# Kernel optimization log

Measured on AMD Instinct MI355X. Metric: run time of the kernel, lower is better.

Reference implementation:

```python
import jax, jax.numpy as jnp
import numpy as np

B, M, D, H, DH = 4, 2048, 1024, 16, 64
R_ATTN, FFN_D, R_FFN = 32, 4096, 512
ROPE_THETA = 10000.0
LN_EPS = 1e-5


def layernorm(x, w, b):
    mu = jnp.mean(x, axis=-1, keepdims=True)
    var = jnp.mean(jnp.square(x - mu), axis=-1, keepdims=True)
    return (x - mu) * jax.lax.rsqrt(var + LN_EPS) * w + b


def headwise_svd(x, U, V, b):
    # x: [B,M,D]; U: [H,D,r]; V: [H,r,dh] -> [B,M,H,dh]
    xr = jnp.einsum('bmd,hdr->bmhr', x, U)
    y = jnp.einsum('bmhr,hrk->bmhk', xr, V)
    return y + b.reshape(U.shape[0], -1)


def rotate_half(x):
    x1, x2 = jnp.split(x, 2, axis=-1)
    return jnp.concatenate([-x2, x1], axis=-1)


def rope_cos_sin(m, dh, dtype):
    inv_freq = 1.0 / (ROPE_THETA ** (jnp.arange(0, dh, 2, dtype=jnp.float32) / dh))
    freqs = jnp.arange(m, dtype=jnp.float32)[:, None] * inv_freq[None, :]  # [M, dh/2]
    emb = jnp.concatenate([freqs, freqs], axis=-1)  # [M, dh]
    return jnp.cos(emb).astype(dtype), jnp.sin(emb).astype(dtype)


def setup_inputs() -> dict:
    key = jax.random.key(0)
    ks = jax.random.split(key, 16)
    s = 0.02
    def n(k, shape, scale=s):
        return jax.random.normal(k, shape, dtype=jnp.float32) * scale
    return dict(
        hidden_states=jax.random.normal(ks[0], (B, M, D), dtype=jnp.float32),
        attention_mask=jnp.ones((B, M), dtype=jnp.int32),
        ln1_w=jnp.ones((D,), jnp.float32), ln1_b=jnp.zeros((D,), jnp.float32),
        Uq=n(ks[1], (H, D, R_ATTN)), Vq=n(ks[2], (H, R_ATTN, DH)), bq=jnp.zeros((D,), jnp.float32),
        Uk=n(ks[3], (H, D, R_ATTN)), Vk=n(ks[4], (H, R_ATTN, DH)), bk=jnp.zeros((D,), jnp.float32),
        Uv=n(ks[5], (H, D, R_ATTN)), Vv=n(ks[6], (H, R_ATTN, DH)), bv=jnp.zeros((D,), jnp.float32),
        Wo_attn=n(ks[7], (D, D)), bo_attn=jnp.zeros((D,), jnp.float32),
        ln2_w=jnp.ones((D,), jnp.float32), ln2_b=jnp.zeros((D,), jnp.float32),
        U_wi=n(ks[8], (D, R_FFN)), V_wi=n(ks[9], (R_FFN, 2 * FFN_D)), b_wi=jnp.zeros((2 * FFN_D,), jnp.float32),
        U_wo=n(ks[10], (FFN_D, R_FFN)), V_wo=n(ks[11], (R_FFN, D)), b_wo=jnp.zeros((D,), jnp.float32),
    )


def reference(hidden_states, attention_mask, ln1_w, ln1_b,
              Uq, Vq, bq, Uk, Vk, bk, Uv, Vv, bv,
              Wo_attn, bo_attn, ln2_w, ln2_b,
              U_wi, V_wi, b_wi, U_wo, V_wo, b_wo):
    x = hidden_states
    xn = layernorm(x, ln1_w, ln1_b)

    # head-wise low-rank SVD QKV projections -> [B,H,M,dh]
    q = headwise_svd(xn, Uq, Vq, bq).transpose(0, 2, 1, 3)
    k = headwise_svd(xn, Uk, Vk, bk).transpose(0, 2, 1, 3)
    v = headwise_svd(xn, Uv, Vv, bv).transpose(0, 2, 1, 3)

    cos, sin = rope_cos_sin(x.shape[1], q.shape[-1], q.dtype)  # [M, dh], broadcasts
    q = q * cos + rotate_half(q) * sin
    k = k * cos + rotate_half(k) * sin

    scale = 1.0 / jnp.sqrt(jnp.asarray(q.shape[-1], q.dtype))
    scores = jnp.einsum('bhqd,bhkd->bhqk', q, k) * scale
    pad = (attention_mask == 0)[:, None, None, :]  # [B,1,1,M]
    scores = jnp.where(pad, jnp.finfo(scores.dtype).min, scores)
    attn = jax.nn.softmax(scores, axis=-1)
    ctx = jnp.einsum('bhqk,bhkd->bhqd', attn, v)
    ctx = ctx.transpose(0, 2, 1, 3).reshape(x.shape)  # [B,M,D]
    attn_out = jnp.einsum('bmd,ed->bme', ctx, Wo_attn) + bo_attn  # dense Wo (torch Linear)
    x = x + attn_out

    # FFN: low-rank Wi -> GEGLU(tanh) -> low-rank Wo
    xn2 = layernorm(x, ln2_w, ln2_b)
    h = (xn2 @ U_wi) @ V_wi + b_wi  # [B,M,2*FFN_D]
    h1, h2 = jnp.split(h, 2, axis=-1)
    g = jax.nn.gelu(h1, approximate=True) * h2  # GEGLU, tanh approx
    ffn_out = (g @ U_wo) @ V_wo + b_wo
    return x + ffn_out
```

## Files before the change

kernel.cpp:

```cpp
#include <hip/hip_runtime.h>
#include <cstdint>

#define DEV __device__ __forceinline__

typedef __attribute__((ext_vector_type(8))) short bf16x8;
typedef __attribute__((ext_vector_type(4))) float f32x4;
typedef __attribute__((ext_vector_type(16))) float f32x16;

#define MFMA(a,b,c) __builtin_amdgcn_mfma_f32_16x16x32_bf16((a),(b),(c),0,0,0)
#define MFMA32(a,b,c) __builtin_amdgcn_mfma_f32_32x32x16_bf16((a),(b),(c),0,0,0)

DEV unsigned short f2bf(float f) {
  union { float f; unsigned u; } v; v.f = f;
  unsigned r = v.u + 0x7fffu + ((v.u >> 16) & 1u);
  return (unsigned short)(r >> 16);
}
DEV float bf2f(unsigned short s) {
  union { unsigned u; float f; } v; v.u = ((unsigned)s) << 16; return v.f;
}
DEV float max3f(float a, float b, float c) { return fmaxf(fmaxf(a, b), c); }

DEV void gload16(const unsigned short* g, short* l) {
  __builtin_amdgcn_global_load_lds(
      (const __attribute__((address_space(1))) unsigned*)g,
      (__attribute__((address_space(3))) unsigned*)l, 16, 0, 0);
}


__global__ __launch_bounds__(256) void k_build_wqkv(
    const float* __restrict__ Uq, const float* __restrict__ Vq,
    const float* __restrict__ Uk, const float* __restrict__ Vk,
    const float* __restrict__ Uv, const float* __restrict__ Vv,
    unsigned short* __restrict__ W) {
  __shared__ float Vl[32 * 64];
  int bx = blockIdx.x;
  int proj = bx >> 6;
  int rem = bx & 63;
  int h = rem >> 2, dblk = rem & 3;
  int tid = threadIdx.x;
  int d = dblk * 256 + tid;
  const float* U = (proj == 0) ? Uq : (proj == 1) ? Uk : Uv;
  const float* V = (proj == 0) ? Vq : (proj == 1) ? Vk : Vv;
  {
    const float4* src = (const float4*)(V + (size_t)h * 2048);
    float4* dst = (float4*)Vl;
    dst[tid] = src[tid];
    dst[tid + 256] = src[tid + 256];
  }
  float u[32];
  {
    const float4* ur = (const float4*)(U + ((size_t)h * 1024 + d) * 32);
#pragma unroll
    for (int q = 0; q < 8; ++q) {
      float4 v = ur[q];
      u[q * 4] = v.x; u[q * 4 + 1] = v.y; u[q * 4 + 2] = v.z; u[q * 4 + 3] = v.w;
    }
  }
  __syncthreads();
  unsigned short* wbase = W + ((size_t)(proj * 1024 + h * 64)) * 1024 + d;
  for (int k = 0; k < 64; ++k) {
    float s = 0.f;
#pragma unroll
    for (int r = 0; r < 32; ++r) s += u[r] * Vl[r * 64 + k];
    wbase[(size_t)k * 1024] = f2bf(s);
  }
}

__global__ void k_concat_bias(const float* __restrict__ bq, const float* __restrict__ bk,
                              const float* __restrict__ bv, float* __restrict__ out) {
  int i = blockIdx.x * 256 + threadIdx.x;
  if (i < 1024) out[i] = bq[i];
  else if (i < 2048) out[i] = bk[i - 1024];
  else if (i < 3072) out[i] = bv[i - 2048];
}

__global__ void k_f2bf(const float* __restrict__ in, unsigned short* __restrict__ out, int n) {
  int i = blockIdx.x * 256 + threadIdx.x;
  if (i < n) out[i] = f2bf(in[i]);
}

__global__ void k_transpose_bf16(const float* __restrict__ in, unsigned short* __restrict__ out,
                                 int R, int C) {
  __shared__ float tile[32][33];
  int c0 = blockIdx.x * 32, r0 = blockIdx.y * 32;
  int tx = threadIdx.x, ty = threadIdx.y;
#pragma unroll
  for (int i = ty; i < 32; i += 8)
    tile[i][tx] = in[(size_t)(r0 + i) * C + c0 + tx];
  __syncthreads();
#pragma unroll
  for (int i = ty; i < 32; i += 8)
    out[(size_t)(c0 + i) * R + r0 + tx] = f2bf(tile[tx][i]);
}

__global__ __launch_bounds__(256) void k_vtrans(const unsigned short* __restrict__ qkv,
                                                unsigned short* __restrict__ vT) {
  __shared__ short t[64][66];
  int bh = blockIdx.y, b = bh >> 4, h = bh & 15;
  int m0 = blockIdx.x << 6;
  int tid = threadIdx.x;
  int rr = tid >> 2, cc = (tid & 3) << 4;
  const unsigned short* src = qkv + ((size_t)(b * 2048 + m0 + rr)) * 3072 + 2048 + h * 64 + cc;
  *(bf16x8*)&t[rr][cc] = *(const bf16x8*)src;
  *(bf16x8*)&t[rr][cc + 8] = *(const bf16x8*)(src + 8);
  __syncthreads();
  unsigned short* dst = vT + ((size_t)bh * 64 + rr) * 2048 + m0 + cc;
  bf16x8 o0, o1;
#pragma unroll
  for (int j = 0; j < 8; ++j) o0[j] = t[cc + j][rr];
#pragma unroll
  for (int j = 0; j < 8; ++j) o1[j] = t[cc + 8 + j][rr];
  *(bf16x8*)dst = o0;
  *(bf16x8*)(dst + 8) = o1;
}

__global__ __launch_bounds__(256) void k_layernorm(const float* __restrict__ x,
                                                   const float* __restrict__ w,
                                                   const float* __restrict__ b,
                                                   unsigned short* __restrict__ out) {
  int row = blockIdx.x;
  int tid = threadIdx.x;
  int lane = tid & 63, wid = tid >> 6;
  const float4 v = ((const float4*)(x + (size_t)row * 1024))[tid];
  float s = v.x + v.y + v.z + v.w;
  float s2 = v.x * v.x + v.y * v.y + v.z * v.z + v.w * v.w;
#pragma unroll
  for (int o = 1; o < 64; o <<= 1) { s += __shfl_xor(s, o); s2 += __shfl_xor(s2, o); }
  __shared__ float as_[4], as2_[4];
  if (lane == 0) { as_[wid] = s; as2_[wid] = s2; }
  __syncthreads();
  s = as_[0] + as_[1] + as_[2] + as_[3];
  s2 = as2_[0] + as2_[1] + as2_[2] + as2_[3];
  float mean = s * (1.f / 1024.f);
  float var = s2 * (1.f / 1024.f) - mean * mean;
  float inv = rsqrtf(var + 1e-5f);
  const float4 wv = ((const float4*)w)[tid];
  const float4 bv = ((const float4*)b)[tid];
  union { unsigned short u[4]; unsigned long long ll; } o;
  o.u[0] = f2bf((v.x - mean) * inv * wv.x + bv.x);
  o.u[1] = f2bf((v.y - mean) * inv * wv.y + bv.y);
  o.u[2] = f2bf((v.z - mean) * inv * wv.z + bv.z);
  o.u[3] = f2bf((v.w - mean) * inv * wv.w + bv.w);
  ((unsigned long long*)(out + (size_t)row * 1024))[tid] = o.ll;
}

template <int EPI>
__global__ __launch_bounds__(256, 2) void k_gemm(const unsigned short* __restrict__ A,
                                                 const unsigned short* __restrict__ Bt,
                                                 const float* __restrict__ bias,
                                                 const float* __restrict__ resid,
                                                 void* __restrict__ outp, int N, int K) {
  __shared__ short Al[128 * 32];
  __shared__ short Bl[128 * 32];
  int tid = threadIdx.x, lane = tid & 63, wid = tid >> 6;
  int wr = wid >> 1, wc = wid & 1;
  size_t row0 = (size_t)blockIdx.y * 128;
  int col0 = blockIdx.x * 128;
  int arow = lane >> 2, acol = (lane & 3) << 3;
  const unsigned short* Ag = A + (row0 + wid * 32 + arow) * K + acol;
  const unsigned short* Bg = Bt + ((size_t)(col0 + wid * 32 + arow)) * K + acol;
  short* Ald = Al + wid * 1024;
  short* Bld = Bl + wid * 1024;
  f32x4 acc[4][4] = {};
  int fr = lane & 15, fk = (lane >> 4) << 3;
  for (int k0 = 0; k0 < K; k0 += 32) {
    __syncthreads();
    gload16(Ag + k0, Ald);
    gload16(Ag + (size_t)16 * K + k0, Ald + 512);
    gload16(Bg + k0, Bld);
    gload16(Bg + (size_t)16 * K + k0, Bld + 512);
    __syncthreads();
    bf16x8 af[4], bfr[4];
#pragma unroll
    for (int i = 0; i < 4; ++i) {
      af[i] = *(const bf16x8*)&Al[(wr * 64 + i * 16 + fr) * 32 + fk];
      bfr[i] = *(const bf16x8*)&Bl[(wc * 64 + i * 16 + fr) * 32 + fk];
    }
#pragma unroll
    for (int i = 0; i < 4; ++i)
#pragma unroll
      for (int j = 0; j < 4; ++j) acc[i][j] = MFMA(af[i], bfr[j], acc[i][j]);
  }
  int cr = (lane >> 4) << 2, cc = lane & 15;
  if (EPI == 3) {
    int c3base = col0 + wc * 64;
    int proj = c3base >> 10;
    unsigned short* out = (unsigned short*)outp;
    if (proj == 2) {
#pragma unroll
      for (int j = 0; j < 4; ++j) {
        int col = c3base + j * 16 + cc;
        float bb = bias[col];
#pragma unroll
        for (int i = 0; i < 4; ++i)
#pragma unroll
          for (int r = 0; r < 4; ++r) {
            size_t row = row0 + wr * 64 + i * 16 + cr + r;
            out[row * N + col] = f2bf(acc[i][j][r] + bb);
          }
      }
    } else {
      float sc = (proj == 0) ? 0.18033688011112042f : 1.f;
#pragma unroll
      for (int jp = 0; jp < 2; ++jp) {
        int irot = jp * 16 + cc;
        float freq = __expf((float)irot * -0.28782313662425575f);
        float bb1 = bias[c3base + jp * 16 + cc];
        float bb2 = bias[c3base + (jp + 2) * 16 + cc];
#pragma unroll
        for (int i = 0; i < 4; ++i)
#pragma unroll
          for (int r = 0; r < 4; ++r) {
            size_t row = row0 + wr * 64 + i * 16 + cr + r;
            int m = (int)(row & 2047);
            float x1v = acc[i][jp][r] + bb1;
            float x2v = acc[i][jp + 2][r] + bb2;
            float sn, csn;
            __sincosf((float)m * freq, &sn, &csn);
            out[row * N + c3base + jp * 16 + cc] = f2bf((x1v * csn - x2v * sn) * sc);
            out[row * N + c3base + (jp + 2) * 16 + cc] = f2bf((x2v * csn + x1v * sn) * sc);
          }
      }
    }
  } else {
#pragma unroll
    for (int j = 0; j < 4; ++j) {
      int col = col0 + wc * 64 + j * 16 + cc;
      float bb = (EPI >= 1) ? bias[col] : 0.f;
#pragma unroll
      for (int i = 0; i < 4; ++i) {
#pragma unroll
        for (int r = 0; r < 4; ++r) {
          size_t row = row0 + wr * 64 + i * 16 + cr + r;
          float v = acc[i][j][r] + bb;
          if (EPI == 2)
            ((float*)outp)[row * N + col] = v + resid[row * N + col];
          else
            ((unsigned short*)outp)[row * N + col] = f2bf(v);
        }
      }
    }
  }
}

__global__ __launch_bounds__(256, 2) void k_gemm_geglu(const unsigned short* __restrict__ A,
                                                       const unsigned short* __restrict__ Bt,
                                                       const float* __restrict__ bias,
                                                       unsigned short* __restrict__ out) {
  __shared__ short Al[128 * 32];
  __shared__ short B1l[128 * 32];
  __shared__ short B2l[128 * 32];
  const int K = 512;
  int tid = threadIdx.x, lane = tid & 63, wid = tid >> 6;
  int wr = wid >> 1, wc = wid & 1;
  size_t row0 = (size_t)blockIdx.y * 128;
  int col0 = blockIdx.x * 128;
  int arow = lane >> 2, acol = (lane & 3) << 3;
  const unsigned short* Ag = A + (row0 + wid * 32 + arow) * K + acol;
  const unsigned short* B1g = Bt + ((size_t)(col0 + wid * 32 + arow)) * K + acol;
  const unsigned short* B2g = Bt + ((size_t)(col0 + 4096 + wid * 32 + arow)) * K + acol;
  short* Ald = Al + wid * 1024;
  short* B1d = B1l + wid * 1024;
  short* B2d = B2l + wid * 1024;
  f32x4 acc1[4][4] = {}, acc2[4][4] = {};
  int fr = lane & 15, fk = (lane >> 4) << 3;
  for (int k0 = 0; k0 < K; k0 += 32) {
    __syncthreads();
    gload16(Ag + k0, Ald);
    gload16(Ag + (size_t)16 * K + k0, Ald + 512);
    gload16(B1g + k0, B1d);
    gload16(B1g + (size_t)16 * K + k0, B1d + 512);
    gload16(B2g + k0, B2d);
    gload16(B2g + (size_t)16 * K + k0, B2d + 512);
    __syncthreads();
    bf16x8 af[4], b1f[4], b2f[4];
#pragma unroll
    for (int i = 0; i < 4; ++i) {
      af[i] = *(const bf16x8*)&Al[(wr * 64 + i * 16 + fr) * 32 + fk];
      b1f[i] = *(const bf16x8*)&B1l[(wc * 64 + i * 16 + fr) * 32 + fk];
      b2f[i] = *(const bf16x8*)&B2l[(wc * 64 + i * 16 + fr) * 32 + fk];
    }
#pragma unroll
    for (int i = 0; i < 4; ++i)
#pragma unroll
      for (int j = 0; j < 4; ++j) {
        acc1[i][j] = MFMA(af[i], b1f[j], acc1[i][j]);
        acc2[i][j] = MFMA(af[i], b2f[j], acc2[i][j]);
      }
  }
  int cr = (lane >> 4) << 2, cc = lane & 15;
#pragma unroll
  for (int j = 0; j < 4; ++j) {
    int col = col0 + wc * 64 + j * 16 + cc;
    float bb1 = bias[col], bb2 = bias[col + 4096];
#pragma unroll
    for (int i = 0; i < 4; ++i) {
#pragma unroll
      for (int r = 0; r < 4; ++r) {
        size_t row = row0 + wr * 64 + i * 16 + cr + r;
        float h1 = acc1[i][j][r] + bb1;
        float h2 = acc2[i][j][r] + bb2;
        float u = 0.7978845608028654f * (h1 + 0.044715f * h1 * h1 * h1);
        float e = __expf(2.f * u);
        float th = 1.f - 2.f / (e + 1.f);
        float gv = 0.5f * h1 * (1.f + th) * h2;
        out[row * 4096 + col] = f2bf(gv);
      }
    }
  }
}

#define KIX(r, c) ((r) * 64 + ((c) ^ (((r) & 7) << 3)))

__global__ __launch_bounds__(256, 4) void k_attn(const unsigned short* __restrict__ qkv,
                                                 const unsigned short* __restrict__ vT,
                                                 const int* __restrict__ mask,
                                                 unsigned short* __restrict__ ctx) {
  __shared__ short Kl[64 * 64];
  __shared__ short Vl[64 * 64];
  __shared__ short Ol[4][32 * 64];
  __shared__ float mpen[64];
  __shared__ int mflag;
  int bh = blockIdx.y, b = bh >> 4, h = bh & 15;
  int q0 = blockIdx.x << 7;
  int tid = threadIdx.x, lane = tid & 63, wid = tid >> 6;
  int qi = lane & 31, hi = lane >> 5;
  const unsigned short* qrow =
      qkv + ((size_t)(b * 2048 + q0 + wid * 32 + qi)) * 3072 + h * 64 + hi * 8;
  bf16x8 qa[4];
#pragma unroll
  for (int c = 0; c < 4; ++c) qa[c] = *(const bf16x8*)(qrow + c * 16);
  float m_r = -1e30f, l_r = 0.f;
  f32x16 oacc0 = {}, oacc1 = {};
  int srw = lane >> 3;
  int schx = ((lane & 7) ^ srw) << 3;
  int rb = wid * 16;
  const unsigned short* kgb =
      qkv + ((size_t)(b * 2048 + rb + srw)) * 3072 + 1024 + h * 64 + schx;
  const unsigned short* vgb = vT + ((size_t)(bh * 64 + rb + srw)) * 2048 + schx;
  short* kld = Kl + rb * 64;
  short* vld = Vl + rb * 64;
  const int* mbase = mask + b * 2048;
  const f32x16 zero16 = {};
  int mv = (tid < 64) ? mbase[tid] : 1;
  for (int k0 = 0; k0 < 2048; k0 += 64) {
    __syncthreads();
    gload16(kgb + (size_t)k0 * 3072, kld);
    gload16(kgb + (size_t)(k0 + 8) * 3072, kld + 512);
    gload16(vgb + k0, vld);
    gload16(vgb + (size_t)8 * 2048 + k0, vld + 512);
    if (wid == 0) {
      mpen[lane] = (mv == 0) ? -1e30f : 0.f;
      unsigned long long bal = __ballot(mv == 0);
      if (lane == 0) mflag = (bal != 0ull) ? 1 : 0;
    }
    if (k0 + 64 < 2048) mv = (tid < 64) ? mbase[k0 + 64 + tid] : 1;
    __syncthreads();
#pragma unroll
    for (int kt = 0; kt < 2; ++kt) {
      f32x16 s = zero16;
      __builtin_amdgcn_s_setprio(1);
#pragma unroll
      for (int c = 0; c < 4; ++c) {
        bf16x8 kf = *(const bf16x8*)&Kl[KIX(kt * 32 + qi, c * 16 + hi * 8)];
        s = MFMA32(kf, qa[c], s);
      }
      __builtin_amdgcn_s_setprio(0);
      if (mflag) {
        const f32x4* mp4 = (const f32x4*)mpen;
#pragma unroll
        for (int t = 0; t < 4; ++t) {
          f32x4 pen = mp4[kt * 8 + t * 2 + hi];
#pragma unroll
          for (int r = 0; r < 4; ++r) s[t * 4 + r] += pen[r];
        }
      }
      float t0 = max3f(s[0], s[1], s[2]);
      float t1 = max3f(s[3], s[4], s[5]);
      float t2 = max3f(s[6], s[7], s[8]);
      float t3 = max3f(s[9], s[10], s[11]);
      float t4 = max3f(s[12], s[13], s[14]);
      float t5 = fmaxf(t0, s[15]);
      float pmax = max3f(max3f(t5, t1, t2), t3, t4);
      pmax = fmaxf(pmax, __shfl_xor(pmax, 32));
      if (!__all(pmax - m_r <= 8.f)) {
        float mn = fmaxf(m_r, pmax);
        float fac = exp2f(m_r - mn);
        m_r = mn;
        l_r *= fac;
#pragma unroll
        for (int r = 0; r < 16; ++r) { oacc0[r] *= fac; oacc1[r] *= fac; }
      }
#pragma unroll
      for (int r = 0; r < 16; ++r) s[r] = exp2f(s[r] - m_r);
      float su0 = (s[0] + s[1]) + (s[2] + s[3]);
      float su1 = (s[4] + s[5]) + (s[6] + s[7]);
      float su2 = (s[8] + s[9]) + (s[10] + s[11]);
      float su3 = (s[12] + s[13]) + (s[14] + s[15]);
      l_r += (su0 + su1) + (su2 + su3);
      unsigned pk[8];
#pragma unroll
      for (int w = 0; w < 8; ++w)
        asm("v_cvt_pk_bf16_f32 %0, %1, %2" : "=v"(pk[w]) : "v"(s[2 * w]), "v"(s[2 * w + 1]));
      unsigned a0 = pk[0], b0 = pk[2];
      unsigned a1 = pk[1], b1 = pk[3];
      unsigned a2 = pk[4], b2 = pk[6];
      unsigned a3 = pk[5], b3 = pk[7];
      asm("v_permlane32_swap_b32 %0, %1" : "+v"(a0), "+v"(b0));
      asm("v_permlane32_swap_b32 %0, %1" : "+v"(a1), "+v"(b1));
      asm("v_permlane32_swap_b32 %0, %1" : "+v"(a2), "+v"(b2));
      asm("v_permlane32_swap_b32 %0, %1" : "+v"(a3), "+v"(b3));
      union { unsigned u[4]; bf16x8 v; } pb0, pb1;
      pb0.u[0] = a0; pb0.u[1] = a1; pb0.u[2] = b0; pb0.u[3] = b1;
      pb1.u[0] = a2; pb1.u[1] = a3; pb1.u[2] = b2; pb1.u[3] = b3;
      __builtin_amdgcn_s_setprio(1);
      {
        bf16x8 vf00 = *(const bf16x8*)&Vl[KIX(qi, kt * 32 + hi * 8)];
        bf16x8 vf01 = *(const bf16x8*)&Vl[KIX(qi, kt * 32 + 16 + hi * 8)];
        oacc0 = MFMA32(vf00, pb0.v, oacc0);
        oacc0 = MFMA32(vf01, pb1.v, oacc0);
        bf16x8 vf10 = *(const bf16x8*)&Vl[KIX(32 + qi, kt * 32 + hi * 8)];
        bf16x8 vf11 = *(const bf16x8*)&Vl[KIX(32 + qi, kt * 32 + 16 + hi * 8)];
        oacc1 = MFMA32(vf10, pb0.v, oacc1);
        oacc1 = MFMA32(vf11, pb1.v, oacc1);
      }
      __builtin_amdgcn_s_setprio(0);
    }
  }
  l_r += __shfl_xor(l_r, 32);
  float invl = 1.f / l_r;
  short* ob = &Ol[wid][0];
  int xsw = (qi & 7) << 3;
#pragma unroll
  for (int t = 0; t < 4; ++t) {
    int d = t * 8 + 4 * hi;
    float a0 = oacc0[4 * t] * invl, a1 = oacc0[4 * t + 1] * invl;
    float a2 = oacc0[4 * t + 2] * invl, a3 = oacc0[4 * t + 3] * invl;
    unsigned w0, w1;
    asm("v_cvt_pk_bf16_f32 %0, %1, %2" : "=v"(w0) : "v"(a0), "v"(a1));
    asm("v_cvt_pk_bf16_f32 %0, %1, %2" : "=v"(w1) : "v"(a2), "v"(a3));
    *(unsigned long long*)&ob[qi * 64 + (d ^ xsw)] =
        ((unsigned long long)w1 << 32) | (unsigned long long)w0;
    float c0 = oacc1[4 * t] * invl, c1 = oacc1[4 * t + 1] * invl;
    float c2 = oacc1[4 * t + 2] * invl, c3 = oacc1[4 * t + 3] * invl;
    unsigned w2, w3;
    asm("v_cvt_pk_bf16_f32 %0, %1, %2" : "=v"(w2) : "v"(c0), "v"(c1));
    asm("v_cvt_pk_bf16_f32 %0, %1, %2" : "=v"(w3) : "v"(c2), "v"(c3));
    *(unsigned long long*)&ob[qi * 64 + ((d + 32) ^ xsw)] =
        ((unsigned long long)w3 << 32) | (unsigned long long)w2;
  }
  __syncthreads();
#pragma unroll
  for (int p = 0; p < 2; ++p) {
    int q = p * 16 + (lane >> 2);
    int qx = (q & 7) << 3;
    unsigned short* dst =
        ctx + ((size_t)(b * 2048 + q0 + wid * 32 + q)) * 1024 + h * 64;
#pragma unroll
    for (int j = 0; j < 2; ++j) {
      int c = (lane & 3) * 8 + j * 32;
      bf16x8 vv = *(const bf16x8*)&ob[q * 64 + (c ^ qx)];
      __builtin_nontemporal_store(vv, (bf16x8*)(dst + c));
    }
  }
}

extern "C" void kernel_launch(void* const* d_in, const int* in_sizes, int n_in, void* d_out,
                              int out_size, void* d_ws, size_t ws_size, hipStream_t stream) {
  const float* x = (const float*)d_in[0];
  const int* amask = (const int*)d_in[1];
  const float* ln1w = (const float*)d_in[2];
  const float* ln1b = (const float*)d_in[3];
  const float* Uq = (const float*)d_in[4];
  const float* Vq = (const float*)d_in[5];
  const float* bq = (const float*)d_in[6];
  const float* Uk = (const float*)d_in[7];
  const float* Vk = (const float*)d_in[8];
  const float* bk = (const float*)d_in[9];
  const float* Uv = (const float*)d_in[10];
  const float* Vv = (const float*)d_in[11];
  const float* bv = (const float*)d_in[12];
  const float* Wo = (const float*)d_in[13];
  const float* bo = (const float*)d_in[14];
  const float* ln2w = (const float*)d_in[15];
  const float* ln2b = (const float*)d_in[16];
  const float* Uwi = (const float*)d_in[17];
  const float* Vwi = (const float*)d_in[18];
  const float* bwi = (const float*)d_in[19];
  const float* Uwo = (const float*)d_in[20];
  const float* Vwo = (const float*)d_in[21];
  const float* bwo = (const float*)d_in[22];

  char* ws = (char*)d_ws;
  size_t off = 0;
  auto alloc = [&](size_t bytes) {
    void* p = ws + off;
    off += (bytes + 255) & ~(size_t)255;
    return p;
  };
  unsigned short* xn = (unsigned short*)alloc((size_t)8192 * 1024 * 2);
  unsigned short* Wqkv = (unsigned short*)alloc((size_t)3072 * 1024 * 2);
  float* bqkv = (float*)alloc(3072 * 4);
  unsigned short* Wob = (unsigned short*)alloc((size_t)1024 * 1024 * 2);
  unsigned short* Uwit = (unsigned short*)alloc((size_t)512 * 1024 * 2);
  unsigned short* Vwit = (unsigned short*)alloc((size_t)8192 * 512 * 2);
  unsigned short* Uwot = (unsigned short*)alloc((size_t)512 * 4096 * 2);
  unsigned short* Vwot = (unsigned short*)alloc((size_t)1024 * 512 * 2);
  unsigned short* qkv = (unsigned short*)alloc((size_t)8192 * 3072 * 2);
  unsigned short* ctx = (unsigned short*)alloc((size_t)8192 * 1024 * 2);
  float* x1 = (float*)alloc((size_t)8192 * 1024 * 4);
  unsigned short* hr = (unsigned short*)alloc((size_t)8192 * 512 * 2);
  unsigned short* gr = (unsigned short*)alloc((size_t)8192 * 512 * 2);
  unsigned short* g = qkv;
  unsigned short* xn2 = xn;
  unsigned short* vT = (unsigned short*)x1;
  if (off > ws_size) return;
  (void)in_sizes; (void)n_in; (void)out_size;

  dim3 tb(32, 8);
  k_build_wqkv<<<192, 256, 0, stream>>>(Uq, Vq, Uk, Vk, Uv, Vv, Wqkv);
  k_concat_bias<<<12, 256, 0, stream>>>(bq, bk, bv, bqkv);
  k_f2bf<<<4096, 256, 0, stream>>>(Wo, Wob, 1024 * 1024);
  k_transpose_bf16<<<dim3(512 / 32, 1024 / 32), tb, 0, stream>>>(Uwi, Uwit, 1024, 512);
  k_transpose_bf16<<<dim3(8192 / 32, 512 / 32), tb, 0, stream>>>(Vwi, Vwit, 512, 8192);
  k_transpose_bf16<<<dim3(512 / 32, 4096 / 32), tb, 0, stream>>>(Uwo, Uwot, 4096, 512);
  k_transpose_bf16<<<dim3(1024 / 32, 512 / 32), tb, 0, stream>>>(Vwo, Vwot, 512, 1024);

  k_layernorm<<<8192, 256, 0, stream>>>(x, ln1w, ln1b, xn);
  k_gemm<3><<<dim3(24, 64), 256, 0, stream>>>(xn, Wqkv, bqkv, nullptr, qkv, 3072, 1024);
  k_vtrans<<<dim3(32, 64), 256, 0, stream>>>(qkv, vT);
  k_attn<<<dim3(16, 64), 256, 0, stream>>>(qkv, vT, amask, ctx);
  k_gemm<2><<<dim3(8, 64), 256, 0, stream>>>(ctx, Wob, bo, x, x1, 1024, 1024);
  k_layernorm<<<8192, 256, 0, stream>>>(x1, ln2w, ln2b, xn2);
  k_gemm<0><<<dim3(4, 64), 256, 0, stream>>>(xn2, Uwit, nullptr, nullptr, hr, 512, 1024);
  k_gemm_geglu<<<dim3(32, 64), 256, 0, stream>>>(hr, Vwit, bwi, g);
  k_gemm<0><<<dim3(4, 64), 256, 0, stream>>>(g, Uwot, nullptr, nullptr, gr, 512, 4096);
  k_gemm<2><<<dim3(8, 64), 256, 0, stream>>>(gr, Vwot, bwo, x1, d_out, 1024, 512);
}
```

Baseline: 530.5 us.

## Compute QKV as low-rank two-stage GEMM instead of materialized dense weight

Replaces the prebuilt dense 3072x1024 QKV weight (U·V) with a fused kernel that first multiplies activations by the transposed U factors (N=1536) and then, per head, multiplies the rank-32 intermediate by V in an MFMA epilogue staged through shared memory, applying bias and RoPE there. This halves the main GEMM's FLOPs and weight traffic and removes the dense weight build kernel. In exchange it adds an extra bf16 rounding of the intermediate, extra LDS use (about 36KB per block for staging), and reads V directly from global memory in the epilogue.

```diff
diff --git a/kernel.cpp b/kernel.cpp
--- a/kernel.cpp
+++ b/kernel.cpp
@@ -27,51 +27,36 @@
 }
 
 
-__global__ __launch_bounds__(256) void k_build_wqkv(
-    const float* __restrict__ Uq, const float* __restrict__ Vq,
-    const float* __restrict__ Uk, const float* __restrict__ Vk,
-    const float* __restrict__ Uv, const float* __restrict__ Vv,
-    unsigned short* __restrict__ W) {
-  __shared__ float Vl[32 * 64];
-  int bx = blockIdx.x;
-  int proj = bx >> 6;
-  int rem = bx & 63;
-  int h = rem >> 2, dblk = rem & 3;
-  int tid = threadIdx.x;
-  int d = dblk * 256 + tid;
+__global__ void k_build_ut(const float* __restrict__ Uq, const float* __restrict__ Uk,
+                           const float* __restrict__ Uv, unsigned short* __restrict__ Ut) {
+  __shared__ float tile[32][33];
+  int s = blockIdx.y;
+  int proj = s >> 4, h = s & 15;
   const float* U = (proj == 0) ? Uq : (proj == 1) ? Uk : Uv;
+  const float* Us = U + (size_t)h * 1024 * 32;
+  int d0 = blockIdx.x * 32;
+  int tx = threadIdx.x, ty = threadIdx.y;
+#pragma unroll
+  for (int i = ty; i < 32; i += 8)
+    tile[i][tx] = Us[(size_t)(d0 + i) * 32 + tx];
+  __syncthreads();
+#pragma unroll
+  for (int i = ty; i < 32; i += 8)
+    Ut[(size_t)(s * 32 + i) * 1024 + d0 + tx] = f2bf(tile[tx][i]);
+}
+
+__global__ void k_build_vt(const float* __restrict__ Vq, const float* __restrict__ Vk,
+                           const float* __restrict__ Vv, unsigned short* __restrict__ Vt) {
+  int ph = blockIdx.x;
+  int proj = ph >> 4, h = ph & 15;
   const float* V = (proj == 0) ? Vq : (proj == 1) ? Vk : Vv;
-  {
-    const float4* src = (const float4*)(V + (size_t)h * 2048);
-    float4* dst = (float4*)Vl;
-    dst[tid] = src[tid];
-    dst[tid + 256] = src[tid + 256];
-  }
-  float u[32];
-  {
-    const float4* ur = (const float4*)(U + ((size_t)h * 1024 + d) * 32);
-#pragma unroll
-    for (int q = 0; q < 8; ++q) {
-      float4 v = ur[q];
-      u[q * 4] = v.x; u[q * 4 + 1] = v.y; u[q * 4 + 2] = v.z; u[q * 4 + 3] = v.w;
-    }
-  }
-  __syncthreads();
-  unsigned short* wbase = W + ((size_t)(proj * 1024 + h * 64)) * 1024 + d;
-  for (int k = 0; k < 64; ++k) {
-    float s = 0.f;
-#pragma unroll
-    for (int r = 0; r < 32; ++r) s += u[r] * Vl[r * 64 + k];
-    wbase[(size_t)k * 1024] = f2bf(s);
-  }
-}
-
-__global__ void k_concat_bias(const float* __restrict__ bq, const float* __restrict__ bk,
-                              const float* __restrict__ bv, float* __restrict__ out) {
-  int i = blockIdx.x * 256 + threadIdx.x;
-  if (i < 1024) out[i] = bq[i];
-  else if (i < 2048) out[i] = bk[i - 1024];
-  else if (i < 3072) out[i] = bv[i - 2048];
+  const float* Vs = V + (size_t)h * 2048;
+  int t = threadIdx.x;
+#pragma unroll
+  for (int idx = t; idx < 2048; idx += 256) {
+    int dh = idx >> 5, r = idx & 31;
+    Vt[(size_t)ph * 2048 + idx] = f2bf(Vs[r * 64 + dh]);
+  }
 }
 
 __global__ void k_f2bf(const float* __restrict__ in, unsigned short* __restrict__ out, int n) {
@@ -182,62 +167,128 @@
       for (int j = 0; j < 4; ++j) acc[i][j] = MFMA(af[i], bfr[j], acc[i][j]);
   }
   int cr = (lane >> 4) << 2, cc = lane & 15;
-  if (EPI == 3) {
-    int c3base = col0 + wc * 64;
-    int proj = c3base >> 10;
-    unsigned short* out = (unsigned short*)outp;
+#pragma unroll
+  for (int j = 0; j < 4; ++j) {
+    int col = col0 + wc * 64 + j * 16 + cc;
+    float bb = (EPI >= 1) ? bias[col] : 0.f;
+#pragma unroll
+    for (int i = 0; i < 4; ++i) {
+#pragma unroll
+      for (int r = 0; r < 4; ++r) {
+        size_t row = row0 + wr * 64 + i * 16 + cr + r;
+        float v = acc[i][j][r] + bb;
+        if (EPI == 2)
+          ((float*)outp)[row * N + col] = v + resid[row * N + col];
+        else
+          ((unsigned short*)outp)[row * N + col] = f2bf(v);
+      }
+    }
+  }
+}
+
+__global__ __launch_bounds__(256, 2) void k_qkv(const unsigned short* __restrict__ A,
+                                                const unsigned short* __restrict__ Ut,
+                                                const unsigned short* __restrict__ Vt,
+                                                const float* __restrict__ bq,
+                                                const float* __restrict__ bk,
+                                                const float* __restrict__ bv,
+                                                unsigned short* __restrict__ qkv) {
+  __shared__ short Al[128 * 32];
+  __shared__ short Bl[128 * 32];
+  __shared__ short Xr[4][64 * 72];
+  const int K = 1024, N3 = 3072;
+  int tid = threadIdx.x, lane = tid & 63, wid = tid >> 6;
+  int wr = wid >> 1, wc = wid & 1;
+  size_t row0 = (size_t)blockIdx.y * 128;
+  int col0 = blockIdx.x * 128;
+  int arow = lane >> 2, acol = (lane & 3) << 3;
+  const unsigned short* Ag = A + (row0 + wid * 32 + arow) * K + acol;
+  const unsigned short* Bg = Ut + ((size_t)(col0 + wid * 32 + arow)) * K + acol;
+  short* Ald = Al + wid * 1024;
+  short* Bld = Bl + wid * 1024;
+  f32x4 acc[4][4] = {};
+  int fr = lane & 15, fk = (lane >> 4) << 3;
+  for (int k0 = 0; k0 < K; k0 += 32) {
+    __syncthreads();
+    gload16(Ag + k0, Ald);
+    gload16(Ag + (size_t)16 * K + k0, Ald + 512);
+    gload16(Bg + k0, Bld);
+    gload16(Bg + (size_t)16 * K + k0, Bld + 512);
+    __syncthreads();
+    bf16x8 af[4], bfr[4];
+#pragma unroll
+    for (int i = 0; i < 4; ++i) {
+      af[i] = *(const bf16x8*)&Al[(wr * 64 + i * 16 + fr) * 32 + fk];
+      bfr[i] = *(const bf16x8*)&Bl[(wc * 64 + i * 16 + fr) * 32 + fk];
+    }
+#pragma unroll
+    for (int i = 0; i < 4; ++i)
+#pragma unroll
+      for (int j = 0; j < 4; ++j) acc[i][j] = MFMA(af[i], bfr[j], acc[i][j]);
+  }
+  int cr = (lane >> 4) << 2, cc = lane & 15;
+  short* xw = &Xr[wid][0];
+#pragma unroll
+  for (int j = 0; j < 4; ++j)
+#pragma unroll
+    for (int i = 0; i < 4; ++i)
+#pragma unroll
+      for (int r = 0; r < 4; ++r)
+        xw[(i * 16 + cr + r) * 72 + j * 16 + cc] = (short)f2bf(acc[i][j][r]);
+  int phbase = blockIdx.x * 4 + wc * 2;
+  const f32x4 zero4 = {0.f, 0.f, 0.f, 0.f};
+#pragma unroll
+  for (int h2 = 0; h2 < 2; ++h2) {
+    int ph = phbase + h2;
+    int proj = ph >> 4, hh = ph & 15;
+    bf16x8 af2[4], bf2[4];
+#pragma unroll
+    for (int i2 = 0; i2 < 4; ++i2)
+      af2[i2] = *(const bf16x8*)&xw[(i2 * 16 + fr) * 72 + h2 * 32 + fk];
+#pragma unroll
+    for (int j2 = 0; j2 < 4; ++j2)
+      bf2[j2] = *(const bf16x8*)(Vt + ((size_t)ph * 64 + j2 * 16 + fr) * 32 + fk);
+    f32x4 a2[4][4];
+#pragma unroll
+    for (int i2 = 0; i2 < 4; ++i2)
+#pragma unroll
+      for (int j2 = 0; j2 < 4; ++j2) a2[i2][j2] = MFMA(af2[i2], bf2[j2], zero4);
+    const float* bp = (proj == 0) ? bq : (proj == 1) ? bk : bv;
+    int obase = proj * 1024 + hh * 64;
     if (proj == 2) {
 #pragma unroll
-      for (int j = 0; j < 4; ++j) {
-        int col = c3base + j * 16 + cc;
-        float bb = bias[col];
-#pragma unroll
-        for (int i = 0; i < 4; ++i)
+      for (int j2 = 0; j2 < 4; ++j2) {
+        int dh = j2 * 16 + cc;
+        float bb = bp[hh * 64 + dh];
+#pragma unroll
+        for (int i2 = 0; i2 < 4; ++i2)
 #pragma unroll
           for (int r = 0; r < 4; ++r) {
-            size_t row = row0 + wr * 64 + i * 16 + cr + r;
-            out[row * N + col] = f2bf(acc[i][j][r] + bb);
+            size_t row = row0 + wr * 64 + i2 * 16 + cr + r;
+            qkv[row * N3 + obase + dh] = f2bf(a2[i2][j2][r] + bb);
           }
       }
     } else {
       float sc = (proj == 0) ? 0.18033688011112042f : 1.f;
 #pragma unroll
-      for (int jp = 0; jp < 2; ++jp) {
-        int irot = jp * 16 + cc;
+      for (int j2 = 0; j2 < 2; ++j2) {
+        int irot = j2 * 16 + cc;
         float freq = __expf((float)irot * -0.28782313662425575f);
-        float bb1 = bias[c3base + jp * 16 + cc];
-        float bb2 = bias[c3base + (jp + 2) * 16 + cc];
-#pragma unroll
-        for (int i = 0; i < 4; ++i)
+        float bb1 = bp[hh * 64 + irot];
+        float bb2 = bp[hh * 64 + irot + 32];
+#pragma unroll
+        for (int i2 = 0; i2 < 4; ++i2)
 #pragma unroll
           for (int r = 0; r < 4; ++r) {
-            size_t row = row0 + wr * 64 + i * 16 + cr + r;
+            size_t row = row0 + wr * 64 + i2 * 16 + cr + r;
             int m = (int)(row & 2047);
-            float x1v = acc[i][jp][r] + bb1;
-            float x2v = acc[i][jp + 2][r] + bb2;
+            float x1v = a2[i2][j2][r] + bb1;
+            float x2v = a2[i2][j2 + 2][r] + bb2;
             float sn, csn;
             __sincosf((float)m * freq, &sn, &csn);
-            out[row * N + c3base + jp * 16 + cc] = f2bf((x1v * csn - x2v * sn) * sc);
-            out[row * N + c3base + (jp + 2) * 16 + cc] = f2bf((x2v * csn + x1v * sn) * sc);
+            qkv[row * N3 + obase + irot] = f2bf((x1v * csn - x2v * sn) * sc);
+            qkv[row * N3 + obase + irot + 32] = f2bf((x2v * csn + x1v * sn) * sc);
           }
-      }
-    }
-  } else {
-#pragma unroll
-    for (int j = 0; j < 4; ++j) {
-      int col = col0 + wc * 64 + j * 16 + cc;
-      float bb = (EPI >= 1) ? bias[col] : 0.f;
-#pragma unroll
-      for (int i = 0; i < 4; ++i) {
-#pragma unroll
-        for (int r = 0; r < 4; ++r) {
-          size_t row = row0 + wr * 64 + i * 16 + cr + r;
-          float v = acc[i][j][r] + bb;
-          if (EPI == 2)
-            ((float*)outp)[row * N + col] = v + resid[row * N + col];
-          else
-            ((unsigned short*)outp)[row * N + col] = f2bf(v);
-        }
       }
     }
   }
@@ -499,8 +550,8 @@
     return p;
   };
   unsigned short* xn = (unsigned short*)alloc((size_t)8192 * 1024 * 2);
-  unsigned short* Wqkv = (unsigned short*)alloc((size_t)3072 * 1024 * 2);
-  float* bqkv = (float*)alloc(3072 * 4);
+  unsigned short* Ut = (unsigned short*)alloc((size_t)1536 * 1024 * 2);
+  unsigned short* Vt = (unsigned short*)alloc((size_t)48 * 2048 * 2);
   unsigned short* Wob = (unsigned short*)alloc((size_t)1024 * 1024 * 2);
   unsigned short* Uwit = (unsigned short*)alloc((size_t)512 * 1024 * 2);
   unsigned short* Vwit = (unsigned short*)alloc((size_t)8192 * 512 * 2);
@@ -518,8 +569,8 @@
   (void)in_sizes; (void)n_in; (void)out_size;
 
   dim3 tb(32, 8);
-  k_build_wqkv<<<192, 256, 0, stream>>>(Uq, Vq, Uk, Vk, Uv, Vv, Wqkv);
-  k_concat_bias<<<12, 256, 0, stream>>>(bq, bk, bv, bqkv);
+  k_build_ut<<<dim3(32, 48), tb, 0, stream>>>(Uq, Uk, Uv, Ut);
+  k_build_vt<<<48, 256, 0, stream>>>(Vq, Vk, Vv, Vt);
   k_f2bf<<<4096, 256, 0, stream>>>(Wo, Wob, 1024 * 1024);
   k_transpose_bf16<<<dim3(512 / 32, 1024 / 32), tb, 0, stream>>>(Uwi, Uwit, 1024, 512);
   k_transpose_bf16<<<dim3(8192 / 32, 512 / 32), tb, 0, stream>>>(Vwi, Vwit, 512, 8192);
@@ -527,7 +578,7 @@
   k_transpose_bf16<<<dim3(1024 / 32, 512 / 32), tb, 0, stream>>>(Vwo, Vwot, 512, 1024);
 
   k_layernorm<<<8192, 256, 0, stream>>>(x, ln1w, ln1b, xn);
-  k_gemm<3><<<dim3(24, 64), 256, 0, stream>>>(xn, Wqkv, bqkv, nullptr, qkv, 3072, 1024);
+  k_qkv<<<dim3(12, 64), 256, 0, stream>>>(xn, Ut, Vt, bq, bk, bv, qkv);
   k_vtrans<<<dim3(32, 64), 256, 0, stream>>>(qkv, vT);
   k_attn<<<dim3(16, 64), 256, 0, stream>>>(qkv, vT, amask, ctx);
   k_gemm<2><<<dim3(8, 64), 256, 0, stream>>>(ctx, Wob, bo, x, x1, 1024, 1024);
```

Result: faster. 485.7 us (-8.4%).
